# Kernel tuning notes

Measured on AMD Instinct MI355X. Metric: run time of the kernel, lower is better.

## Reference

```python
import jax, jax.numpy as jnp
import numpy as np

N = 50000
E = 250000
NUM_ETYPES = 4
H = 2  # num_heads
EPS = 1e-12


def _gat_conv(x, W, al, ar, b, src, dst):
    # x: (N, in_dim); W: (in_dim, H*D); al/ar/b: (H, D); src/dst: (E,)
    D = al.shape[-1]
    feat = (x @ W).reshape(-1, H, D)            # (N, H, D)
    el = jnp.sum(feat * al, axis=-1)            # (N, H)
    er = jnp.sum(feat * ar, axis=-1)            # (N, H)
    e = jax.nn.leaky_relu(el[src] + er[dst], 0.2)   # (E, H)
    emax = jax.ops.segment_max(e, dst, num_segments=N)
    ex = jnp.exp(e - emax[dst])
    denom = jax.ops.segment_sum(ex, dst, num_segments=N)
    alpha = ex / denom[dst]                     # (E, H) segment softmax over in-edges
    msg = feat[src] * alpha[:, :, None]         # (E, H, D)
    out = jax.ops.segment_sum(msg, dst, num_segments=N)  # (N, H, D)
    return out + b


def _hetero_layer(x, W, al, ar, b, edges):
    # vmap GATConv over the edge-type axis, then HeteroGraphConv aggregate='mean'
    outs = jax.vmap(lambda w, a, r, bb, e: _gat_conv(x, w, a, r, bb, e[0], e[1]))(
        W, al, ar, b, edges)                    # (T, N, H, D)
    return jnp.mean(outs, axis=0)               # (N, H, D)


def _post(v):
    # relu -> F.normalize(dim=1, i.e. across heads) -> dropout(eval: identity) -> mean over heads
    v = jax.nn.relu(v)
    norm = jnp.sqrt(jnp.sum(v * v, axis=1, keepdims=True))
    v = v / jnp.maximum(norm, EPS)
    return jnp.mean(v, axis=1)                  # (N, D)


def setup_inputs() -> dict:
    key = jax.random.key(0)
    ks = jax.random.split(key, 16)
    s = 0.05
    inp = {
        'x': jax.random.normal(ks[0], (N, 23), jnp.float32),
        'edges': jax.random.randint(ks[1], (NUM_ETYPES, 2, E), 0, N, jnp.int32),
        'W0': jax.random.normal(ks[2], (NUM_ETYPES, 23, H * 64), jnp.float32) * s,
        'al0': jax.random.normal(ks[3], (NUM_ETYPES, H, 64), jnp.float32) * s,
        'ar0': jax.random.normal(ks[4], (NUM_ETYPES, H, 64), jnp.float32) * s,
        'b0': jnp.zeros((NUM_ETYPES, H, 64), jnp.float32),
        'W1': jax.random.normal(ks[5], (NUM_ETYPES, 64, H * 64), jnp.float32) * s,
        'al1': jax.random.normal(ks[6], (NUM_ETYPES, H, 64), jnp.float32) * s,
        'ar1': jax.random.normal(ks[7], (NUM_ETYPES, H, 64), jnp.float32) * s,
        'b1': jnp.zeros((NUM_ETYPES, H, 64), jnp.float32),
        'W2': jax.random.normal(ks[8], (NUM_ETYPES, 64, H * 64), jnp.float32) * s,
        'al2': jax.random.normal(ks[9], (NUM_ETYPES, H, 64), jnp.float32) * s,
        'ar2': jax.random.normal(ks[10], (NUM_ETYPES, H, 64), jnp.float32) * s,
        'b2': jnp.zeros((NUM_ETYPES, H, 64), jnp.float32),
    }
    return inp


def reference(x, edges, W0, al0, ar0, b0, W1, al1, ar1, b1, W2, al2, ar2, b2):
    h = x  # feature_by_level, feat_level=0
    h = _post(_hetero_layer(h, W0, al0, ar0, b0, edges))
    h = _post(_hetero_layer(h, W1, al1, ar1, b1, edges))
    h = jnp.mean(_hetero_layer(h, W2, al2, ar2, b2, edges), axis=1)  # (N, out_dim)
    out = jnp.mean(h, axis=0, keepdims=True)    # dgl.mean_nodes, single graph -> (1, out_dim)
    return out
```

## Files before the change

### kernel.cpp

```cpp
#include <hip/hip_runtime.h>

#define NN 50000
#define NE 250000
#define NSCAN_BLKS ((NN + 255)/256)
#define EDGE_BLKS ((4*NE + 255)/256)
#define NBUCK 4
#define BSZ ((NN + NBUCK - 1)/NBUCK)

typedef __attribute__((ext_vector_type(8))) short bf16x8;
typedef __attribute__((ext_vector_type(4))) float f32x4;

__device__ inline ushort f2bf(float f) {
  uint u = __float_as_uint(f);
  return (ushort)((u + 0x7fffu + ((u >> 16) & 1u)) >> 16);
}
__device__ inline float bf2f(ushort b) { return __uint_as_float(((uint)b) << 16); }

__global__ __launch_bounds__(256) void zero_ints(int* __restrict__ p, int n) {
  int i = blockIdx.x*256 + threadIdx.x;
  if (i < n) p[i] = 0;
}
__global__ __launch_bounds__(256) void zero_floats(float* __restrict__ p, int n) {
  int i = blockIdx.x*256 + threadIdx.x;
  if (i < n) p[i] = 0.f;
}

__global__ __launch_bounds__(256) void count_kernel(const int* __restrict__ edges, int* __restrict__ counts) {
  int idx = blockIdx.x*256 + threadIdx.x;
  if (idx >= 4*NE) return;
  int t = idx / NE, e = idx - t*NE;
  int dst = edges[(size_t)t*2*NE + NE + e];
  atomicAdd(&counts[t*NN + dst], 1);
}

__global__ __launch_bounds__(256) void sumdeg_kernel(const int* __restrict__ counts, int* __restrict__ totdeg) {
  int v = blockIdx.x*256 + threadIdx.x;
  if (v < NN) totdeg[v] = counts[v] + counts[NN+v] + counts[2*NN+v] + counts[3*NN+v];
}

__global__ __launch_bounds__(256) void scan1_kernel(const int* __restrict__ in, int* __restrict__ out, int* __restrict__ bsum, int n) {
  __shared__ int sd[256];
  int i = blockIdx.x*256 + threadIdx.x;
  int v = (i < n) ? in[i] : 0;
  sd[threadIdx.x] = v;
  __syncthreads();
  for (int off = 1; off < 256; off <<= 1) {
    int add = (threadIdx.x >= off) ? sd[threadIdx.x - off] : 0;
    __syncthreads();
    sd[threadIdx.x] += add;
    __syncthreads();
  }
  if (i < n) out[i] = sd[threadIdx.x] - v;
  if (threadIdx.x == 255) bsum[blockIdx.x] = sd[255];
}

__global__ __launch_bounds__(1024) void scan2_kernel(int* __restrict__ bsum, int nb) {
  __shared__ int sd[1024];
  int i = threadIdx.x;
  int v = (i < nb) ? bsum[i] : 0;
  sd[i] = v;
  __syncthreads();
  for (int off = 1; off < 1024; off <<= 1) {
    int add = (i >= off) ? sd[i - off] : 0;
    __syncthreads();
    sd[i] += add;
    __syncthreads();
  }
  if (i < nb) bsum[i] = sd[i] - v;
}

__global__ __launch_bounds__(256) void scan3b_kernel(int* __restrict__ rp, const int* __restrict__ bsum, int n, int total) {
  int i = blockIdx.x*256 + threadIdx.x;
  if (i < n) rp[i] += bsum[blockIdx.x];
  if (i == 0) rp[n] = total;
}

__global__ __launch_bounds__(256) void make_cursor_kernel(const int* __restrict__ rp2, const int* __restrict__ counts,
                                                          int* __restrict__ cursor, int* __restrict__ sub_ptr) {
  int v = blockIdx.x*256 + threadIdx.x;
  if (v >= NN) return;
  int b = rp2[v];
  int s1 = b  + counts[v];
  int s2 = s1 + counts[NN+v];
  int s3 = s2 + counts[2*NN+v];
  cursor[v] = b; cursor[NN+v] = s1; cursor[2*NN+v] = s2; cursor[3*NN+v] = s3;
  sub_ptr[NN+v] = s1; sub_ptr[2*NN+v] = s2; sub_ptr[3*NN+v] = s3;
}

__global__ __launch_bounds__(256) void scatter_bucketed(const int* __restrict__ edges, int* __restrict__ cursor,
                                                        int* __restrict__ col2) {
  const int b = blockIdx.x / EDGE_BLKS;
  const int idx = (blockIdx.x - b*EDGE_BLKS)*256 + threadIdx.x;
  if (idx >= 4*NE) return;
  const int t = idx / NE, e = idx - t*NE;
  const int dst = edges[(size_t)t*2*NE + NE + e];
  if (dst < b*BSZ || dst >= (b+1)*BSZ) return;
  const int src = edges[(size_t)t*2*NE + e];
  const int pos = atomicAdd(&cursor[t*NN + dst], 1);
  col2[pos] = src;
}

__global__ __launch_bounds__(256) void convert_x_kernel(const float* __restrict__ x, ushort* __restrict__ xpad) {
  int i = blockIdx.x*256 + threadIdx.x;
  if (i >= NN*64) return;
  int k = i & 63, n = i >> 6;
  xpad[i] = (k < 23) ? f2bf(x[n*23 + k]) : (ushort)0;
}

__global__ __launch_bounds__(256) void convert_wb_kernel(const float* __restrict__ W, ushort* __restrict__ WB, int Kin) {
  int i = blockIdx.x*256 + threadIdx.x;
  if (i >= 4*128*64) return;
  int k = i & 63, c = (i >> 6) & 127, t = i >> 13;
  float w = (k < Kin) ? W[((size_t)t*Kin + k)*128 + c] : 0.f;
  WB[i] = f2bf(w);
}

__global__ __launch_bounds__(256) void walwar_kernel(const float* __restrict__ W, const float* __restrict__ al,
                                                     const float* __restrict__ ar, ushort* __restrict__ wwb, int Kin) {
  int i = blockIdx.x*256 + threadIdx.x;
  if (i >= 16*64) return;
  int c = i >> 6, k = i & 63;
  int lr = c >> 3, t = (c >> 1) & 3, h = c & 1;
  float v = 0.f;
  if (k < Kin) {
    const float* A = (lr ? ar : al) + t*128 + h*64;
    const float* wr = W + ((size_t)t*Kin + k)*128 + h*64;
    for (int d = 0; d < 64; ++d) v += wr[d]*A[d];
  }
  wwb[i] = f2bf(v);
}

__global__ __launch_bounds__(256)
void elk_kernel(const ushort* __restrict__ hbf, const ushort* __restrict__ wwb,
                float* __restrict__ elp, float* __restrict__ erp)
{
  __shared__ ushort BS[16*64];
  __shared__ float sC[16*66];
  const int tid = threadIdx.x;
  if (tid < 128) ((bf16x8*)BS)[tid] = ((const bf16x8*)wwb)[tid];
  __syncthreads();

  const int wv = tid >> 6, lane = tid & 63;
  const int mrow = lane & 15, kq = lane >> 4;
  const int anode = blockIdx.x*64 + wv*16 + mrow;

  const bf16x8 a0 = *(const bf16x8*)(hbf + (size_t)anode*64 + kq*8);
  const bf16x8 a1 = *(const bf16x8*)(hbf + (size_t)anode*64 + 32 + kq*8);
  const bf16x8 b0 = *(const bf16x8*)(BS + mrow*64 + kq*8);
  const bf16x8 b1 = *(const bf16x8*)(BS + mrow*64 + 32 + kq*8);

  f32x4 acc = (f32x4){0.f,0.f,0.f,0.f};
  acc = __builtin_amdgcn_mfma_f32_16x16x32_bf16(a0, b0, acc, 0, 0, 0);
  acc = __builtin_amdgcn_mfma_f32_16x16x32_bf16(a1, b1, acc, 0, 0, 0);

  #pragma unroll
  for (int r = 0; r < 4; ++r) sC[mrow*66 + wv*16 + kq*4 + r] = acc[r];
  __syncthreads();

  const int t = tid >> 6, n = tid & 63;
  const int node = blockIdx.x*64 + n;
  if (node < NN) {
    float2 e2 = make_float2(sC[(t*2+0)*66 + n], sC[(t*2+1)*66 + n]);
    float2 r2 = make_float2(sC[(8+t*2+0)*66 + n], sC[(8+t*2+1)*66 + n]);
    ((float2*)elp)[(size_t)t*NN + node] = e2;
    ((float2*)erp)[(size_t)t*NN + node] = r2;
  }
}

__global__ __launch_bounds__(256)
void gather_kernel(const ushort* __restrict__ hbf, const float* __restrict__ elp,
                   const float* __restrict__ erp, const int* __restrict__ col2,
                   const int* __restrict__ row_ptr2, const int* __restrict__ sub_ptr,
                   ushort* __restrict__ agg)
{
  const int v = __builtin_amdgcn_readfirstlane(blockIdx.x*4 + (threadIdx.x >> 6));
  const int lane = threadIdx.x & 63;
  const int h2 = lane >> 5;
  const int j  = lane & 31;
  const uint* hb32 = (const uint*)hbf;
  uint* agg32 = (uint*)agg;

  const int b0 = row_ptr2[v];
  const int b4 = row_ptr2[v+1];
  const int s1 = sub_ptr[NN+v], s2 = sub_ptr[2*NN+v], s3 = sub_ptr[3*NN+v];
  const int bounds[5] = {b0, s1, s2, s3, b4};

  #pragma unroll
  for (int t = 0; t < 4; ++t) {
    const int lo = bounds[t], hi = bounds[t+1];
    float ox = 0.f, oy = 0.f;
    if (lo < hi) {
      const float2 er2 = ((const float2*)erp)[(size_t)t*NN + v];
      float sum0 = 0.f, sum1 = 0.f, tx0 = 0.f, ty0 = 0.f, tx1 = 0.f, ty1 = 0.f;
      #pragma unroll 2
      for (int q = lo + h2; q < hi; q += 2) {
        const int src = col2[q];
        const float2 e2 = ((const float2*)elp)[(size_t)t*NN + src];
        float u0 = e2.x + er2.x, u1 = e2.y + er2.y;
        u0 = (u0 > 0.f) ? u0 : 0.2f*u0;
        u1 = (u1 > 0.f) ? u1 : 0.2f*u1;
        const float p0 = __expf(fminf(u0, 80.f));
        const float p1 = __expf(fminf(u1, 80.f));
        sum0 += p0; sum1 += p1;
        const uint w = hb32[(uint)src*32u + (uint)j];
        const float xv0 = __uint_as_float(w << 16);
        const float xv1 = __uint_as_float(w & 0xffff0000u);
        tx0 += p0*xv0; ty0 += p0*xv1;
        tx1 += p1*xv0; ty1 += p1*xv1;
      }
      sum0 += __shfl_xor(sum0, 32); sum1 += __shfl_xor(sum1, 32);
      tx0 += __shfl_xor(tx0, 32);   ty0 += __shfl_xor(ty0, 32);
      tx1 += __shfl_xor(tx1, 32);   ty1 += __shfl_xor(ty1, 32);
      const float i0 = __builtin_amdgcn_rcpf(sum0);
      const float i1 = __builtin_amdgcn_rcpf(sum1);
      ox = h2 ? tx1*i1 : tx0*i0;
      oy = h2 ? ty1*i1 : ty0*i0;
    }
    const uint pk = (uint)f2bf(ox) | ((uint)f2bf(oy) << 16);
    __builtin_nontemporal_store(pk, &agg32[(size_t)(t*NN + v)*64 + h2*32 + j]);
  }
}

__global__ __launch_bounds__(256)
void transform_kernel(const ushort* __restrict__ agg, const ushort* __restrict__ WB,
                      const float* __restrict__ ball, ushort* __restrict__ hout, int post)
{
  __shared__ ushort WT[2*128*64];
  __shared__ float sb[128];
  const int tid = threadIdx.x;
  if (tid < 128) sb[tid] = 0.25f*(ball[tid] + ball[128+tid] + ball[256+tid] + ball[384+tid]);

  const int wv = tid >> 6, lane = tid & 63;
  const int mrow = lane & 15, kq = lane >> 4;
  const int node0 = blockIdx.x*64;
  const int anode = node0 + wv*16 + mrow;

  f32x4 acc[8];
  #pragma unroll
  for (int nb = 0; nb < 8; ++nb) acc[nb] = (f32x4){0.f,0.f,0.f,0.f};

  for (int tb = 0; tb < 4; tb += 2) {
    __syncthreads();
    for (int i = tid; i < 2048; i += 256) {
      int row = i >> 3, jj = i & 7;
      bf16x8 val = ((const bf16x8*)WB)[tb*1024 + i];
      *(bf16x8*)((char*)WT + row*128 + ((jj ^ (row & 7))*16)) = val;
    }
    __syncthreads();
    #pragma unroll
    for (int t2 = 0; t2 < 2; ++t2) {
      const int t = tb + t2;
      const ushort* ar_ = agg + ((size_t)t*NN + anode)*128;
      const bf16x8 a00 = __builtin_nontemporal_load((const bf16x8*)(ar_ + kq*8));
      const bf16x8 a01 = __builtin_nontemporal_load((const bf16x8*)(ar_ + 32 + kq*8));
      const bf16x8 a10 = __builtin_nontemporal_load((const bf16x8*)(ar_ + 64 + kq*8));
      const bf16x8 a11 = __builtin_nontemporal_load((const bf16x8*)(ar_ + 96 + kq*8));
      #pragma unroll
      for (int nb = 0; nb < 8; ++nb) {
        const int row = t2*128 + nb*16 + mrow;
        const bf16x8 b0 = *(const bf16x8*)((const char*)WT + row*128 + ((kq       ^ (row&7))*16));
        const bf16x8 b1 = *(const bf16x8*)((const char*)WT + row*128 + (((4 + kq) ^ (row&7))*16));
        acc[nb] = __builtin_amdgcn_mfma_f32_16x16x32_bf16(nb < 4 ? a00 : a10, b0, acc[nb], 0, 0, 0);
        acc[nb] = __builtin_amdgcn_mfma_f32_16x16x32_bf16(nb < 4 ? a01 : a11, b1, acc[nb], 0, 0, 0);
      }
    }
  }

  const int noder = node0 + wv*16 + kq*4;
  #pragma unroll
  for (int nb = 0; nb < 4; ++nb) {
    const int d = nb*16 + mrow;
    const float bm0 = sb[d], bm1 = sb[64 + d];
    #pragma unroll
    for (int r = 0; r < 4; ++r) {
      if (noder + r < NN) {
        float h0 = 0.25f*acc[nb][r]   + bm0;
        float h1 = 0.25f*acc[nb+4][r] + bm1;
        float o;
        if (post) {
          h0 = fmaxf(h0, 0.f); h1 = fmaxf(h1, 0.f);
          o = 0.5f*(h0 + h1) / fmaxf(sqrtf(h0*h0 + h1*h1), 1e-12f);
        } else {
          o = 0.5f*(h0 + h1);
        }
        hout[(size_t)(noder + r)*64 + d] = f2bf(o);
      }
    }
  }
}

__global__ __launch_bounds__(256) void reduce_nodes(const ushort* __restrict__ hn, float* __restrict__ accum) {
  __shared__ float sd[256];
  int d = threadIdx.x & 63, rg = threadIdx.x >> 6;
  float s = 0.f;
  for (int r = blockIdx.x*4 + rg; r < NN; r += gridDim.x*4) s += bf2f(hn[(size_t)r*64 + d]);
  sd[threadIdx.x] = s;
  __syncthreads();
  if (threadIdx.x < 64) {
    s = sd[threadIdx.x] + sd[threadIdx.x+64] + sd[threadIdx.x+128] + sd[threadIdx.x+192];
    atomicAdd(&accum[threadIdx.x], s);
  }
}
__global__ __launch_bounds__(64) void final_out_kernel(const float* __restrict__ accum, float* __restrict__ out) {
  int d = threadIdx.x;
  if (d < 64) out[d] = accum[d] * (1.0f/NN);
}

extern "C" void kernel_launch(void* const* d_in, const int* in_sizes, int n_in,
                              void* d_out, int out_size, void* d_ws, size_t ws_size,
                              hipStream_t stream) {
  const float* x     = (const float*)d_in[0];
  const int*   edges = (const int*)d_in[1];
  const float* W[3]  = {(const float*)d_in[2], (const float*)d_in[6], (const float*)d_in[10]};
  const float* al[3] = {(const float*)d_in[3], (const float*)d_in[7], (const float*)d_in[11]};
  const float* ar[3] = {(const float*)d_in[4], (const float*)d_in[8], (const float*)d_in[12]};
  const float* b[3]  = {(const float*)d_in[5], (const float*)d_in[9], (const float*)d_in[13]};

  char* ws = (char*)d_ws;
  auto up = [](size_t x_) { return (x_ + 255) & ~(size_t)255; };

  const size_t szAgg  = ((size_t)4*NN + 64)*128*sizeof(ushort);
  const size_t szElp  = (size_t)4*NN*2*sizeof(float);
  const size_t szHB   = (size_t)(NN+64)*64*sizeof(ushort);
  const size_t szWB   = (size_t)4*128*64*sizeof(ushort);
  const size_t szWWB  = (size_t)16*64*sizeof(ushort);
  const size_t szCol  = (size_t)4*NE*sizeof(int);
  const size_t szI4   = (size_t)4*NN*sizeof(int);
  const size_t szI1   = (size_t)(NN+1)*sizeof(int);

  size_t o = 0;
  ushort* agg    = (ushort*)(ws + o); o += up(szAgg);
  float*  elp    = (float*)(ws + o);  o += up(szElp);
  float*  erp    = (float*)(ws + o);  o += up(szElp);
  ushort* xpad   = (ushort*)(ws + o); o += up(szHB);
  ushort* hbuf   = (ushort*)(ws + o); o += up(szHB);
  ushort* WB     = (ushort*)(ws + o); o += up(szWB);
  ushort* wwb    = (ushort*)(ws + o); o += up(szWWB);
  float*  accum  = (float*)(ws + o);  o += up(256);
  int*    col2   = (int*)(ws + o);    o += up(szCol);
  int* row_ptr2  = (int*)(ws + o);    o += up(szI1);
  int* totdeg    = (int*)(ws + o);    o += up(szI1);
  int* cursor    = (int*)(ws + o);    o += up(szI4);
  int* counts    = (int*)(ws + o);    o += up(szI4);
  int* sub_ptr   = (int*)(ws + o);    o += up(szI4);
  int* bsum      = (int*)(ws + o);    o += up(4096);

  zero_ints<<<(4*NN + 255)/256, 256, 0, stream>>>(counts, 4*NN);
  count_kernel<<<EDGE_BLKS, 256, 0, stream>>>(edges, counts);
  sumdeg_kernel<<<NSCAN_BLKS, 256, 0, stream>>>(counts, totdeg);
  scan1_kernel<<<NSCAN_BLKS, 256, 0, stream>>>(totdeg, row_ptr2, bsum, NN);
  scan2_kernel<<<1, 1024, 0, stream>>>(bsum, NSCAN_BLKS);
  scan3b_kernel<<<NSCAN_BLKS, 256, 0, stream>>>(row_ptr2, bsum, NN, 4*NE);
  make_cursor_kernel<<<NSCAN_BLKS, 256, 0, stream>>>(row_ptr2, counts, cursor, sub_ptr);
  scatter_bucketed<<<NBUCK*EDGE_BLKS, 256, 0, stream>>>(edges, cursor, col2);

  convert_x_kernel<<<(NN*64 + 255)/256, 256, 0, stream>>>(x, xpad);

  const int gemmGX = (NN + 63)/64;

  for (int l = 0; l < 3; ++l) {
    const ushort* hin = (l == 0) ? xpad : hbuf;
    const int Kin = (l == 0) ? 23 : 64;
    convert_wb_kernel<<<(4*128*64 + 255)/256, 256, 0, stream>>>(W[l], WB, Kin);
    walwar_kernel<<<(16*64 + 255)/256, 256, 0, stream>>>(W[l], al[l], ar[l], wwb, Kin);
    elk_kernel<<<gemmGX, 256, 0, stream>>>(hin, wwb, elp, erp);
    gather_kernel<<<NN/4, 256, 0, stream>>>(hin, elp, erp, col2, row_ptr2, sub_ptr, agg);
    transform_kernel<<<gemmGX, 256, 0, stream>>>(agg, WB, b[l], hbuf, (l < 2) ? 1 : 0);
  }

  zero_floats<<<1, 64, 0, stream>>>(accum, 64);
  reduce_nodes<<<256, 256, 0, stream>>>(hbuf, accum);
  final_out_kernel<<<1, 64, 0, stream>>>(accum, (float*)d_out);
}
```

Measured before the change: 396.7 us.

## Precompute per-edge attention exponentials in separate kernel; drop LDS staging in transform

```diff
diff --git a/kernel.cpp b/kernel.cpp
--- a/kernel.cpp
+++ b/kernel.cpp
@@ -4,7 +4,7 @@
 #define NE 250000
 #define NSCAN_BLKS ((NN + 255)/256)
 #define EDGE_BLKS ((4*NE + 255)/256)
-#define NBUCK 4
+#define NBUCK 8
 #define BSZ ((NN + NBUCK - 1)/NBUCK)
 
 typedef __attribute__((ext_vector_type(8))) short bf16x8;
@@ -88,7 +88,7 @@
 }
 
 __global__ __launch_bounds__(256) void scatter_bucketed(const int* __restrict__ edges, int* __restrict__ cursor,
-                                                        int* __restrict__ col2) {
+                                                        int2* __restrict__ cd2) {
   const int b = blockIdx.x / EDGE_BLKS;
   const int idx = (blockIdx.x - b*EDGE_BLKS)*256 + threadIdx.x;
   if (idx >= 4*NE) return;
@@ -97,7 +97,7 @@
   if (dst < b*BSZ || dst >= (b+1)*BSZ) return;
   const int src = edges[(size_t)t*2*NE + e];
   const int pos = atomicAdd(&cursor[t*NN + dst], 1);
-  col2[pos] = src;
+  cd2[pos] = make_int2(t*NN + src, t*NN + dst);
 }
 
 __global__ __launch_bounds__(256) void convert_x_kernel(const float* __restrict__ x, ushort* __restrict__ xpad) {
@@ -168,10 +168,24 @@
 }
 
 __global__ __launch_bounds__(256)
-void gather_kernel(const ushort* __restrict__ hbf, const float* __restrict__ elp,
-                   const float* __restrict__ erp, const int* __restrict__ col2,
-                   const int* __restrict__ row_ptr2, const int* __restrict__ sub_ptr,
-                   ushort* __restrict__ agg)
+void pexp_kernel(const int2* __restrict__ cd2, const float* __restrict__ elp,
+                 const float* __restrict__ erp, float2* __restrict__ pexp2)
+{
+  int q = blockIdx.x*256 + threadIdx.x;
+  if (q >= 4*NE) return;
+  const int2 cd = cd2[q];
+  const float2 e2 = ((const float2*)elp)[cd.x];
+  const float2 r2 = ((const float2*)erp)[cd.y];
+  float u0 = e2.x + r2.x, u1 = e2.y + r2.y;
+  u0 = (u0 > 0.f) ? u0 : 0.2f*u0;
+  u1 = (u1 > 0.f) ? u1 : 0.2f*u1;
+  pexp2[q] = make_float2(__expf(fminf(u0, 80.f)), __expf(fminf(u1, 80.f)));
+}
+
+__global__ __launch_bounds__(256)
+void gather_kernel(const ushort* __restrict__ hbf, const float2* __restrict__ pexp2,
+                   const int2* __restrict__ cd2, const int* __restrict__ row_ptr2,
+                   const int* __restrict__ sub_ptr, ushort* __restrict__ agg)
 {
   const int v = __builtin_amdgcn_readfirstlane(blockIdx.x*4 + (threadIdx.x >> 6));
   const int lane = threadIdx.x & 63;
@@ -188,25 +202,20 @@
   #pragma unroll
   for (int t = 0; t < 4; ++t) {
     const int lo = bounds[t], hi = bounds[t+1];
+    const int tbase = t*NN;
     float ox = 0.f, oy = 0.f;
     if (lo < hi) {
-      const float2 er2 = ((const float2*)erp)[(size_t)t*NN + v];
       float sum0 = 0.f, sum1 = 0.f, tx0 = 0.f, ty0 = 0.f, tx1 = 0.f, ty1 = 0.f;
-      #pragma unroll 2
+      #pragma unroll 4
       for (int q = lo + h2; q < hi; q += 2) {
-        const int src = col2[q];
-        const float2 e2 = ((const float2*)elp)[(size_t)t*NN + src];
-        float u0 = e2.x + er2.x, u1 = e2.y + er2.y;
-        u0 = (u0 > 0.f) ? u0 : 0.2f*u0;
-        u1 = (u1 > 0.f) ? u1 : 0.2f*u1;
-        const float p0 = __expf(fminf(u0, 80.f));
-        const float p1 = __expf(fminf(u1, 80.f));
-        sum0 += p0; sum1 += p1;
+        const float2 pp = pexp2[q];
+        const int src = cd2[q].x - tbase;
         const uint w = hb32[(uint)src*32u + (uint)j];
         const float xv0 = __uint_as_float(w << 16);
         const float xv1 = __uint_as_float(w & 0xffff0000u);
-        tx0 += p0*xv0; ty0 += p0*xv1;
-        tx1 += p1*xv0; ty1 += p1*xv1;
+        sum0 += pp.x; sum1 += pp.y;
+        tx0 += pp.x*xv0; ty0 += pp.x*xv1;
+        tx1 += pp.y*xv0; ty1 += pp.y*xv1;
       }
       sum0 += __shfl_xor(sum0, 32); sum1 += __shfl_xor(sum1, 32);
       tx0 += __shfl_xor(tx0, 32);   ty0 += __shfl_xor(ty0, 32);
@@ -217,7 +226,7 @@
       oy = h2 ? ty1*i1 : ty0*i0;
     }
     const uint pk = (uint)f2bf(ox) | ((uint)f2bf(oy) << 16);
-    __builtin_nontemporal_store(pk, &agg32[(size_t)(t*NN + v)*64 + h2*32 + j]);
+    __builtin_nontemporal_store(pk, &agg32[(size_t)(tbase + v)*64 + h2*32 + j]);
   }
 }
 
@@ -225,11 +234,7 @@
 void transform_kernel(const ushort* __restrict__ agg, const ushort* __restrict__ WB,
                       const float* __restrict__ ball, ushort* __restrict__ hout, int post)
 {
-  __shared__ ushort WT[2*128*64];
-  __shared__ float sb[128];
   const int tid = threadIdx.x;
-  if (tid < 128) sb[tid] = 0.25f*(ball[tid] + ball[128+tid] + ball[256+tid] + ball[384+tid]);
-
   const int wv = tid >> 6, lane = tid & 63;
   const int mrow = lane & 15, kq = lane >> 4;
   const int node0 = blockIdx.x*64;
@@ -239,30 +244,21 @@
   #pragma unroll
   for (int nb = 0; nb < 8; ++nb) acc[nb] = (f32x4){0.f,0.f,0.f,0.f};
 
-  for (int tb = 0; tb < 4; tb += 2) {
-    __syncthreads();
-    for (int i = tid; i < 2048; i += 256) {
-      int row = i >> 3, jj = i & 7;
-      bf16x8 val = ((const bf16x8*)WB)[tb*1024 + i];
-      *(bf16x8*)((char*)WT + row*128 + ((jj ^ (row & 7))*16)) = val;
-    }
-    __syncthreads();
+  #pragma unroll
+  for (int t = 0; t < 4; ++t) {
+    const ushort* ar_ = agg + ((size_t)t*NN + anode)*128;
+    const bf16x8 a00 = __builtin_nontemporal_load((const bf16x8*)(ar_ + kq*8));
+    const bf16x8 a01 = __builtin_nontemporal_load((const bf16x8*)(ar_ + 32 + kq*8));
+    const bf16x8 a10 = __builtin_nontemporal_load((const bf16x8*)(ar_ + 64 + kq*8));
+    const bf16x8 a11 = __builtin_nontemporal_load((const bf16x8*)(ar_ + 96 + kq*8));
+    const ushort* wb_t = WB + (size_t)t*128*64;
     #pragma unroll
-    for (int t2 = 0; t2 < 2; ++t2) {
-      const int t = tb + t2;
-      const ushort* ar_ = agg + ((size_t)t*NN + anode)*128;
-      const bf16x8 a00 = __builtin_nontemporal_load((const bf16x8*)(ar_ + kq*8));
-      const bf16x8 a01 = __builtin_nontemporal_load((const bf16x8*)(ar_ + 32 + kq*8));
-      const bf16x8 a10 = __builtin_nontemporal_load((const bf16x8*)(ar_ + 64 + kq*8));
-      const bf16x8 a11 = __builtin_nontemporal_load((const bf16x8*)(ar_ + 96 + kq*8));
-      #pragma unroll
-      for (int nb = 0; nb < 8; ++nb) {
-        const int row = t2*128 + nb*16 + mrow;
-        const bf16x8 b0 = *(const bf16x8*)((const char*)WT + row*128 + ((kq       ^ (row&7))*16));
-        const bf16x8 b1 = *(const bf16x8*)((const char*)WT + row*128 + (((4 + kq) ^ (row&7))*16));
-        acc[nb] = __builtin_amdgcn_mfma_f32_16x16x32_bf16(nb < 4 ? a00 : a10, b0, acc[nb], 0, 0, 0);
-        acc[nb] = __builtin_amdgcn_mfma_f32_16x16x32_bf16(nb < 4 ? a01 : a11, b1, acc[nb], 0, 0, 0);
-      }
+    for (int nb = 0; nb < 8; ++nb) {
+      const int c = nb*16 + mrow;
+      const bf16x8 b0 = *(const bf16x8*)(wb_t + c*64 + kq*8);
+      const bf16x8 b1 = *(const bf16x8*)(wb_t + c*64 + 32 + kq*8);
+      acc[nb] = __builtin_amdgcn_mfma_f32_16x16x32_bf16(nb < 4 ? a00 : a10, b0, acc[nb], 0, 0, 0);
+      acc[nb] = __builtin_amdgcn_mfma_f32_16x16x32_bf16(nb < 4 ? a01 : a11, b1, acc[nb], 0, 0, 0);
     }
   }
 
@@ -270,7 +266,8 @@
   #pragma unroll
   for (int nb = 0; nb < 4; ++nb) {
     const int d = nb*16 + mrow;
-    const float bm0 = sb[d], bm1 = sb[64 + d];
+    const float bm0 = 0.25f*(ball[d]      + ball[128+d]      + ball[256+d]      + ball[384+d]);
+    const float bm1 = 0.25f*(ball[64+d]   + ball[192+d]      + ball[320+d]      + ball[448+d]);
     #pragma unroll
     for (int r = 0; r < 4; ++r) {
       if (noder + r < NN) {
@@ -324,7 +321,8 @@
   const size_t szHB   = (size_t)(NN+64)*64*sizeof(ushort);
   const size_t szWB   = (size_t)4*128*64*sizeof(ushort);
   const size_t szWWB  = (size_t)16*64*sizeof(ushort);
-  const size_t szCol  = (size_t)4*NE*sizeof(int);
+  const size_t szCd2  = (size_t)4*NE*sizeof(int2);
+  const size_t szPex  = (size_t)4*NE*sizeof(float2);
   const size_t szI4   = (size_t)4*NN*sizeof(int);
   const size_t szI1   = (size_t)(NN+1)*sizeof(int);
 
@@ -337,7 +335,8 @@
   ushort* WB     = (ushort*)(ws + o); o += up(szWB);
   ushort* wwb    = (ushort*)(ws + o); o += up(szWWB);
   float*  accum  = (float*)(ws + o);  o += up(256);
-  int*    col2   = (int*)(ws + o);    o += up(szCol);
+  int2*   cd2    = (int2*)(ws + o);   o += up(szCd2);
+  float2* pexp2  = (float2*)(ws + o); o += up(szPex);
   int* row_ptr2  = (int*)(ws + o);    o += up(szI1);
   int* totdeg    = (int*)(ws + o);    o += up(szI1);
   int* cursor    = (int*)(ws + o);    o += up(szI4);
@@ -352,7 +351,7 @@
   scan2_kernel<<<1, 1024, 0, stream>>>(bsum, NSCAN_BLKS);
   scan3b_kernel<<<NSCAN_BLKS, 256, 0, stream>>>(row_ptr2, bsum, NN, 4*NE);
   make_cursor_kernel<<<NSCAN_BLKS, 256, 0, stream>>>(row_ptr2, counts, cursor, sub_ptr);
-  scatter_bucketed<<<NBUCK*EDGE_BLKS, 256, 0, stream>>>(edges, cursor, col2);
+  scatter_bucketed<<<NBUCK*EDGE_BLKS, 256, 0, stream>>>(edges, cursor, cd2);
 
   convert_x_kernel<<<(NN*64 + 255)/256, 256, 0, stream>>>(x, xpad);
 
@@ -364,7 +363,8 @@
     convert_wb_kernel<<<(4*128*64 + 255)/256, 256, 0, stream>>>(W[l], WB, Kin);
     walwar_kernel<<<(16*64 + 255)/256, 256, 0, stream>>>(W[l], al[l], ar[l], wwb, Kin);
     elk_kernel<<<gemmGX, 256, 0, stream>>>(hin, wwb, elp, erp);
-    gather_kernel<<<NN/4, 256, 0, stream>>>(hin, elp, erp, col2, row_ptr2, sub_ptr, agg);
+    pexp_kernel<<<EDGE_BLKS, 256, 0, stream>>>(cd2, elp, erp, pexp2);
+    gather_kernel<<<NN/4, 256, 0, stream>>>(hin, pexp2, cd2, row_ptr2, sub_ptr, agg);
     transform_kernel<<<gemmGX, 256, 0, stream>>>(agg, WB, b[l], hbuf, (l < 2) ? 1 : 0);
   }
 
```

New measurement: 490.5 us. 1.24x slower.

## Fuse edge gather-softmax aggregation with per-type MFMA transform in shared memory

Applied to the files above, without the earlier changes.

```diff
diff --git a/kernel.cpp b/kernel.cpp
--- a/kernel.cpp
+++ b/kernel.cpp
@@ -168,125 +168,115 @@
 }
 
 __global__ __launch_bounds__(256)
-void gather_kernel(const ushort* __restrict__ hbf, const float* __restrict__ elp,
-                   const float* __restrict__ erp, const int* __restrict__ col2,
-                   const int* __restrict__ row_ptr2, const int* __restrict__ sub_ptr,
-                   ushort* __restrict__ agg)
+void fused_gat_kernel(const ushort* __restrict__ hbf, const float* __restrict__ elp,
+                      const float* __restrict__ erp, const int* __restrict__ col2,
+                      const int* __restrict__ row_ptr2, const int* __restrict__ sub_ptr,
+                      const ushort* __restrict__ WB, const float* __restrict__ ball,
+                      ushort* __restrict__ hout, int post)
 {
-  const int v = __builtin_amdgcn_readfirstlane(blockIdx.x*4 + (threadIdx.x >> 6));
-  const int lane = threadIdx.x & 63;
+  __shared__ ushort aggs[4][16][136];
+  __shared__ float  sC[16][132];
+  __shared__ float  sb[128];
+  const int tid = threadIdx.x;
+  const int wv = tid >> 6, lane = tid & 63;
   const int h2 = lane >> 5;
   const int j  = lane & 31;
   const uint* hb32 = (const uint*)hbf;
-  uint* agg32 = (uint*)agg;
-
-  const int b0 = row_ptr2[v];
-  const int b4 = row_ptr2[v+1];
-  const int s1 = sub_ptr[NN+v], s2 = sub_ptr[2*NN+v], s3 = sub_ptr[3*NN+v];
-  const int bounds[5] = {b0, s1, s2, s3, b4};
+
+  if (tid < 128) sb[tid] = 0.25f*(ball[tid] + ball[128+tid] + ball[256+tid] + ball[384+tid]);
+
+  for (int i = 0; i < 4; ++i) {
+    const int vl = wv*4 + i;
+    const int v = __builtin_amdgcn_readfirstlane(blockIdx.x*16 + vl);
+    const int b0 = row_ptr2[v];
+    const int b4 = row_ptr2[v+1];
+    const int s1 = sub_ptr[NN+v], s2 = sub_ptr[2*NN+v], s3 = sub_ptr[3*NN+v];
+    const int bounds[5] = {b0, s1, s2, s3, b4};
+
+    #pragma unroll
+    for (int t = 0; t < 4; ++t) {
+      const int lo = bounds[t], hi = bounds[t+1];
+      float ox = 0.f, oy = 0.f;
+      if (lo < hi) {
+        const float2 er2 = ((const float2*)erp)[(size_t)t*NN + v];
+        float sum0 = 0.f, sum1 = 0.f, tx0 = 0.f, ty0 = 0.f, tx1 = 0.f, ty1 = 0.f;
+        #pragma unroll 2
+        for (int q = lo + h2; q < hi; q += 2) {
+          const int src = col2[q];
+          const float2 e2 = ((const float2*)elp)[(size_t)t*NN + src];
+          float u0 = e2.x + er2.x, u1 = e2.y + er2.y;
+          u0 = (u0 > 0.f) ? u0 : 0.2f*u0;
+          u1 = (u1 > 0.f) ? u1 : 0.2f*u1;
+          const float p0 = __expf(fminf(u0, 80.f));
+          const float p1 = __expf(fminf(u1, 80.f));
+          sum0 += p0; sum1 += p1;
+          const uint w = hb32[(uint)src*32u + (uint)j];
+          const float xv0 = __uint_as_float(w << 16);
+          const float xv1 = __uint_as_float(w & 0xffff0000u);
+          tx0 += p0*xv0; ty0 += p0*xv1;
+          tx1 += p1*xv0; ty1 += p1*xv1;
+        }
+        sum0 += __shfl_xor(sum0, 32); sum1 += __shfl_xor(sum1, 32);
+        tx0 += __shfl_xor(tx0, 32);   ty0 += __shfl_xor(ty0, 32);
+        tx1 += __shfl_xor(tx1, 32);   ty1 += __shfl_xor(ty1, 32);
+        const float i0 = __builtin_amdgcn_rcpf(sum0);
+        const float i1 = __builtin_amdgcn_rcpf(sum1);
+        ox = h2 ? tx1*i1 : tx0*i0;
+        oy = h2 ? ty1*i1 : ty0*i0;
+      }
+      const uint pk = (uint)f2bf(ox) | ((uint)f2bf(oy) << 16);
+      ((uint*)&aggs[t][vl][0])[h2*32 + j] = pk;
+    }
+  }
+  __syncthreads();
+
+  const int mrow = lane & 15, kq = lane >> 4;
+  const int h = wv >> 1;
+  const int colbase = wv*32;
+
+  f32x4 acc[2];
+  acc[0] = (f32x4){0.f,0.f,0.f,0.f};
+  acc[1] = (f32x4){0.f,0.f,0.f,0.f};
 
   #pragma unroll
   for (int t = 0; t < 4; ++t) {
-    const int lo = bounds[t], hi = bounds[t+1];
-    float ox = 0.f, oy = 0.f;
-    if (lo < hi) {
-      const float2 er2 = ((const float2*)erp)[(size_t)t*NN + v];
-      float sum0 = 0.f, sum1 = 0.f, tx0 = 0.f, ty0 = 0.f, tx1 = 0.f, ty1 = 0.f;
-      #pragma unroll 2
-      for (int q = lo + h2; q < hi; q += 2) {
-        const int src = col2[q];
-        const float2 e2 = ((const float2*)elp)[(size_t)t*NN + src];
-        float u0 = e2.x + er2.x, u1 = e2.y + er2.y;
-        u0 = (u0 > 0.f) ? u0 : 0.2f*u0;
-        u1 = (u1 > 0.f) ? u1 : 0.2f*u1;
-        const float p0 = __expf(fminf(u0, 80.f));
-        const float p1 = __expf(fminf(u1, 80.f));
-        sum0 += p0; sum1 += p1;
-        const uint w = hb32[(uint)src*32u + (uint)j];
-        const float xv0 = __uint_as_float(w << 16);
-        const float xv1 = __uint_as_float(w & 0xffff0000u);
-        tx0 += p0*xv0; ty0 += p0*xv1;
-        tx1 += p1*xv0; ty1 += p1*xv1;
-      }
-      sum0 += __shfl_xor(sum0, 32); sum1 += __shfl_xor(sum1, 32);
-      tx0 += __shfl_xor(tx0, 32);   ty0 += __shfl_xor(ty0, 32);
-      tx1 += __shfl_xor(tx1, 32);   ty1 += __shfl_xor(ty1, 32);
-      const float i0 = __builtin_amdgcn_rcpf(sum0);
-      const float i1 = __builtin_amdgcn_rcpf(sum1);
-      ox = h2 ? tx1*i1 : tx0*i0;
-      oy = h2 ? ty1*i1 : ty0*i0;
+    const bf16x8 aA = *(const bf16x8*)&aggs[t][mrow][h*64 + kq*8];
+    const bf16x8 aB = *(const bf16x8*)&aggs[t][mrow][h*64 + 32 + kq*8];
+    const ushort* wb_t = WB + (size_t)t*128*64;
+    #pragma unroll
+    for (int nb = 0; nb < 2; ++nb) {
+      const int c = colbase + nb*16 + mrow;
+      const bf16x8 b0 = *(const bf16x8*)(wb_t + c*64 + kq*8);
+      const bf16x8 b1 = *(const bf16x8*)(wb_t + c*64 + 32 + kq*8);
+      acc[nb] = __builtin_amdgcn_mfma_f32_16x16x32_bf16(aA, b0, acc[nb], 0, 0, 0);
+      acc[nb] = __builtin_amdgcn_mfma_f32_16x16x32_bf16(aB, b1, acc[nb], 0, 0, 0);
     }
-    const uint pk = (uint)f2bf(ox) | ((uint)f2bf(oy) << 16);
-    __builtin_nontemporal_store(pk, &agg32[(size_t)(t*NN + v)*64 + h2*32 + j]);
-  }
-}
-
-__global__ __launch_bounds__(256)
-void transform_kernel(const ushort* __restrict__ agg, const ushort* __restrict__ WB,
-                      const float* __restrict__ ball, ushort* __restrict__ hout, int post)
-{
-  __shared__ ushort WT[2*128*64];
-  __shared__ float sb[128];
-  const int tid = threadIdx.x;
-  if (tid < 128) sb[tid] = 0.25f*(ball[tid] + ball[128+tid] + ball[256+tid] + ball[384+tid]);
-
-  const int wv = tid >> 6, lane = tid & 63;
-  const int mrow = lane & 15, kq = lane >> 4;
-  const int node0 = blockIdx.x*64;
-  const int anode = node0 + wv*16 + mrow;
-
-  f32x4 acc[8];
+  }
   #pragma unroll
-  for (int nb = 0; nb < 8; ++nb) acc[nb] = (f32x4){0.f,0.f,0.f,0.f};
-
-  for (int tb = 0; tb < 4; tb += 2) {
-    __syncthreads();
-    for (int i = tid; i < 2048; i += 256) {
-      int row = i >> 3, jj = i & 7;
-      bf16x8 val = ((const bf16x8*)WB)[tb*1024 + i];
-      *(bf16x8*)((char*)WT + row*128 + ((jj ^ (row & 7))*16)) = val;
+  for (int nb = 0; nb < 2; ++nb)
+    #pragma unroll
+    for (int r = 0; r < 4; ++r)
+      sC[kq*4 + r][colbase + nb*16 + mrow] = acc[nb][r];
+  __syncthreads();
+
+  const int node = tid >> 4, dseg = tid & 15;
+  const int v = blockIdx.x*16 + node;
+  ushort pk4[4];
+  #pragma unroll
+  for (int i = 0; i < 4; ++i) {
+    const int d = dseg*4 + i;
+    float h0 = 0.25f*sC[node][d]      + sb[d];
+    float h1 = 0.25f*sC[node][64 + d] + sb[64 + d];
+    float o;
+    if (post) {
+      h0 = fmaxf(h0, 0.f); h1 = fmaxf(h1, 0.f);
+      o = 0.5f*(h0 + h1) / fmaxf(sqrtf(h0*h0 + h1*h1), 1e-12f);
+    } else {
+      o = 0.5f*(h0 + h1);
     }
-    __syncthreads();
-    #pragma unroll
-    for (int t2 = 0; t2 < 2; ++t2) {
-      const int t = tb + t2;
-      const ushort* ar_ = agg + ((size_t)t*NN + anode)*128;
-      const bf16x8 a00 = __builtin_nontemporal_load((const bf16x8*)(ar_ + kq*8));
-      const bf16x8 a01 = __builtin_nontemporal_load((const bf16x8*)(ar_ + 32 + kq*8));
-      const bf16x8 a10 = __builtin_nontemporal_load((const bf16x8*)(ar_ + 64 + kq*8));
-      const bf16x8 a11 = __builtin_nontemporal_load((const bf16x8*)(ar_ + 96 + kq*8));
-      #pragma unroll
-      for (int nb = 0; nb < 8; ++nb) {
-        const int row = t2*128 + nb*16 + mrow;
-        const bf16x8 b0 = *(const bf16x8*)((const char*)WT + row*128 + ((kq       ^ (row&7))*16));
-        const bf16x8 b1 = *(const bf16x8*)((const char*)WT + row*128 + (((4 + kq) ^ (row&7))*16));
-        acc[nb] = __builtin_amdgcn_mfma_f32_16x16x32_bf16(nb < 4 ? a00 : a10, b0, acc[nb], 0, 0, 0);
-        acc[nb] = __builtin_amdgcn_mfma_f32_16x16x32_bf16(nb < 4 ? a01 : a11, b1, acc[nb], 0, 0, 0);
-      }
-    }
-  }
-
-  const int noder = node0 + wv*16 + kq*4;
-  #pragma unroll
-  for (int nb = 0; nb < 4; ++nb) {
-    const int d = nb*16 + mrow;
-    const float bm0 = sb[d], bm1 = sb[64 + d];
-    #pragma unroll
-    for (int r = 0; r < 4; ++r) {
-      if (noder + r < NN) {
-        float h0 = 0.25f*acc[nb][r]   + bm0;
-        float h1 = 0.25f*acc[nb+4][r] + bm1;
-        float o;
-        if (post) {
-          h0 = fmaxf(h0, 0.f); h1 = fmaxf(h1, 0.f);
-          o = 0.5f*(h0 + h1) / fmaxf(sqrtf(h0*h0 + h1*h1), 1e-12f);
-        } else {
-          o = 0.5f*(h0 + h1);
-        }
-        hout[(size_t)(noder + r)*64 + d] = f2bf(o);
-      }
-    }
-  }
+    pk4[i] = f2bf(o);
+  }
+  *(ushort4*)&hout[(size_t)v*64 + dseg*4] = *(ushort4*)pk4;
 }
 
 __global__ __launch_bounds__(256) void reduce_nodes(const ushort* __restrict__ hn, float* __restrict__ accum) {
@@ -319,7 +309,6 @@
   char* ws = (char*)d_ws;
   auto up = [](size_t x_) { return (x_ + 255) & ~(size_t)255; };
 
-  const size_t szAgg  = ((size_t)4*NN + 64)*128*sizeof(ushort);
   const size_t szElp  = (size_t)4*NN*2*sizeof(float);
   const size_t szHB   = (size_t)(NN+64)*64*sizeof(ushort);
   const size_t szWB   = (size_t)4*128*64*sizeof(ushort);
@@ -329,11 +318,11 @@
   const size_t szI1   = (size_t)(NN+1)*sizeof(int);
 
   size_t o = 0;
-  ushort* agg    = (ushort*)(ws + o); o += up(szAgg);
   float*  elp    = (float*)(ws + o);  o += up(szElp);
   float*  erp    = (float*)(ws + o);  o += up(szElp);
   ushort* xpad   = (ushort*)(ws + o); o += up(szHB);
-  ushort* hbuf   = (ushort*)(ws + o); o += up(szHB);
+  ushort* hbuf0  = (ushort*)(ws + o); o += up(szHB);
+  ushort* hbuf1  = (ushort*)(ws + o); o += up(szHB);
   ushort* WB     = (ushort*)(ws + o); o += up(szWB);
   ushort* wwb    = (ushort*)(ws + o); o += up(szWWB);
   float*  accum  = (float*)(ws + o);  o += up(256);
@@ -358,17 +347,19 @@
 
   const int gemmGX = (NN + 63)/64;
 
+  const ushort* hin = xpad;
+  ushort* houts[3] = {hbuf0, hbuf1, hbuf0};
   for (int l = 0; l < 3; ++l) {
-    const ushort* hin = (l == 0) ? xpad : hbuf;
     const int Kin = (l == 0) ? 23 : 64;
     convert_wb_kernel<<<(4*128*64 + 255)/256, 256, 0, stream>>>(W[l], WB, Kin);
     walwar_kernel<<<(16*64 + 255)/256, 256, 0, stream>>>(W[l], al[l], ar[l], wwb, Kin);
     elk_kernel<<<gemmGX, 256, 0, stream>>>(hin, wwb, elp, erp);
-    gather_kernel<<<NN/4, 256, 0, stream>>>(hin, elp, erp, col2, row_ptr2, sub_ptr, agg);
-    transform_kernel<<<gemmGX, 256, 0, stream>>>(agg, WB, b[l], hbuf, (l < 2) ? 1 : 0);
+    fused_gat_kernel<<<NN/16, 256, 0, stream>>>(hin, elp, erp, col2, row_ptr2, sub_ptr,
+                                                WB, b[l], houts[l], (l < 2) ? 1 : 0);
+    hin = houts[l];
   }
 
   zero_floats<<<1, 64, 0, stream>>>(accum, 64);
-  reduce_nodes<<<256, 256, 0, stream>>>(hbuf, accum);
+  reduce_nodes<<<256, 256, 0, stream>>>(hbuf0, accum);
   final_out_kernel<<<1, 64, 0, stream>>>(accum, (float*)d_out);
 }
```

Measured after the change: 458.7 us. +15.6%, slower.
